# Optimization experiments

Measured on AMD Instinct MI355X. Metric: run time of the kernel, lower is better.

## Reference

```python
import jax, jax.numpy as jnp
import numpy as np

V, C, T_MAX, H, L = 32000, 256, 2048, 8, 4
HS = C // H          # head_size = 32
FFN = 256            # hard-coded in Encoder
CLS_H, N_OUT = 512, 10
B, T = 4, 2048
EPS = 1e-5


def _ln(x, g, b):
    mu = jnp.mean(x, axis=-1, keepdims=True)
    var = jnp.mean(jnp.square(x - mu), axis=-1, keepdims=True)
    return (x - mu) * jax.lax.rsqrt(var + EPS) * g + b


def setup_inputs() -> dict:
    key = jax.random.key(0)
    ks = jax.random.split(key, 16)
    s = 0.02
    return {
        "idx": jax.random.randint(ks[0], (B, T), 0, V),
        "tok_emb": jax.random.normal(ks[1], (V, C), jnp.float32) * s,
        "pos_emb": jax.random.normal(ks[2], (T_MAX, C), jnp.float32) * s,
        "Wq": jax.random.normal(ks[3], (L, H, C, HS), jnp.float32) * s,
        "Wk": jax.random.normal(ks[4], (L, H, C, HS), jnp.float32) * s,
        "Wv": jax.random.normal(ks[5], (L, H, C, HS), jnp.float32) * s,
        "Wproj": jax.random.normal(ks[6], (L, C, C), jnp.float32) * s,
        "bproj": jnp.zeros((L, C), jnp.float32),
        "ln1_g": jnp.ones((L, C), jnp.float32), "ln1_b": jnp.zeros((L, C), jnp.float32),
        "ln2_g": jnp.ones((L, C), jnp.float32), "ln2_b": jnp.zeros((L, C), jnp.float32),
        "W1": jax.random.normal(ks[7], (L, C, FFN), jnp.float32) * s,
        "b1": jnp.zeros((L, FFN), jnp.float32),
        "W2": jax.random.normal(ks[8], (L, FFN, C), jnp.float32) * s,
        "b2": jnp.zeros((L, C), jnp.float32),
        "lnf_g": jnp.ones((C,), jnp.float32), "lnf_b": jnp.zeros((C,), jnp.float32),
        "Wc1": jax.random.normal(ks[9], (C, CLS_H), jnp.float32) * s,
        "bc1": jnp.zeros((CLS_H,), jnp.float32),
        "Wc2": jax.random.normal(ks[10], (CLS_H, N_OUT), jnp.float32) * s,
        "bc2": jnp.zeros((N_OUT,), jnp.float32),
    }


def reference(idx, tok_emb, pos_emb, Wq, Wk, Wv, Wproj, bproj,
              ln1_g, ln1_b, ln2_g, ln2_b, W1, b1, W2, b2,
              lnf_g, lnf_b, Wc1, bc1, Wc2, bc2):
    Bc, Tc = idx.shape
    x = tok_emb[idx] + pos_emb[:Tc]                       # [B,T,C]
    scale = C ** (-0.5)                                   # NOTE: scales by n_embd, not head_size (faithful)
    for i in range(L):
        h = _ln(x, ln1_g[i], ln1_b[i])
        q = jnp.einsum('btc,hcd->bhtd', h, Wq[i])
        k = jnp.einsum('btc,hcd->bhtd', h, Wk[i])
        v = jnp.einsum('btc,hcd->bhtd', h, Wv[i])
        wei = jax.nn.softmax(jnp.einsum('bhtd,bhsd->bhts', q, k) * scale, axis=-1)
        o = jnp.einsum('bhts,bhsd->bhtd', wei, v)         # [B,H,T,HS]
        o = o.transpose(0, 2, 1, 3).reshape(Bc, Tc, C)    # concat heads
        x = x + jnp.einsum('btc,cd->btd', o, Wproj[i]) + bproj[i]
        h2 = _ln(x, ln2_g[i], ln2_b[i])
        f = jax.nn.relu(jnp.einsum('btc,cf->btf', h2, W1[i]) + b1[i])
        x = x + jnp.einsum('btf,fc->btc', f, W2[i]) + b2[i]
    x = _ln(x, lnf_g, lnf_b)
    emb = jnp.mean(x, axis=1)                             # [B,C] mean pool over T
    logits = jax.nn.relu(emb @ Wc1 + bc1) @ Wc2 + bc2
    return jax.nn.softmax(logits, axis=1)                 # [B, n_output]
```

## Files before the change

kernel.cpp:

```cpp
#include <hip/hip_runtime.h>
#include <hip/hip_bf16.h>

#define NTOK 8192
#define CDIM 256
#define TDIM 2048
#define BDIM 4
#define HDIM 8
#define HSZ  32
#define LNUM 4
#define BUF  (NTOK*CDIM)
#define QSTR 768
#define LC   0.0901684400056f

typedef __attribute__((ext_vector_type(8))) short short8v;
typedef __attribute__((ext_vector_type(4))) short short4v;
typedef __attribute__((ext_vector_type(4))) float float4v;

#if __has_builtin(__builtin_amdgcn_cvt_pk_bf16_f32)
static __device__ __forceinline__ unsigned pkbf(float a, float b){
  auto t = __builtin_amdgcn_cvt_pk_bf16_f32(a, b);
  union { decltype(t) v; unsigned u; } cv; cv.v = t;
  return cv.u;
}
static __device__ __forceinline__ short f2bs(float f){
  auto t = __builtin_amdgcn_cvt_pk_bf16_f32(f, f);
  union { decltype(t) v; unsigned u; } cv; cv.v = t;
  return (short)(cv.u & 0xFFFFu);
}
#else
static __device__ __forceinline__ short f2bs(float f){
  union { float f; unsigned u; } x; x.f = f;
  unsigned r = x.u + 0x7FFFu + ((x.u >> 16) & 1u);
  return (short)(r >> 16);
}
static __device__ __forceinline__ unsigned pkbf(float a, float b){
  union { float f; unsigned u; } x, y; x.f = a; y.f = b;
  unsigned ra = x.u + 0x7FFFu + ((x.u >> 16) & 1u);
  unsigned rb = y.u + 0x7FFFu + ((y.u >> 16) & 1u);
  return __builtin_amdgcn_perm(rb, ra, 0x07060302u);
}
#endif
#if __has_builtin(__builtin_amdgcn_exp2f)
static __device__ __forceinline__ float fexp2(float x){ return __builtin_amdgcn_exp2f(x); }
#else
static __device__ __forceinline__ float fexp2(float x){ return __expf(x*0.6931471805599453f); }
#endif

#if __has_builtin(__builtin_amdgcn_mfma_f32_16x16x16bf16_1k)
static __device__ __forceinline__ float4v mfma16(short4v a, short4v b, float4v c){
  return __builtin_amdgcn_mfma_f32_16x16x16bf16_1k(a, b, c, 0, 0, 0);
}
#else
static __device__ __forceinline__ float4v mfma16(short4v a, short4v b, float4v c){
  float4v d;
  asm volatile("v_mfma_f32_16x16x16_bf16 %0, %1, %2, %3\n\ts_nop 7\n\ts_nop 7"
               : "=v"(d) : "v"(a), "v"(b), "v"(c));
  return d;
}
#endif
static __device__ __forceinline__ float4v mfma32(short8v a, short8v b, float4v c){
  return __builtin_amdgcn_mfma_f32_16x16x32_bf16(a, b, c, 0, 0, 0);
}

__global__ __launch_bounds__(256) void k_prep_embed(
    const int* __restrict__ idx, const float* __restrict__ tok, const float* __restrict__ pos,
    const float* __restrict__ Wq, const float* __restrict__ Wk, const float* __restrict__ Wv,
    const float* __restrict__ Wp, const float* __restrict__ W1, const float* __restrict__ W2,
    const float* __restrict__ l1g, const float* __restrict__ l2g,
    const float* __restrict__ l1b, const float* __restrict__ l2b,
    const float* __restrict__ b1, const float* __restrict__ Wc1, const float* __restrict__ lnfg,
    const float* __restrict__ lnfb, const float* __restrict__ bc1,
    short* __restrict__ qkvT, short* __restrict__ wpT, short* __restrict__ w1T, short* __restrict__ w2T,
    float* __restrict__ bq, float* __restrict__ b1f, float* __restrict__ Wc1s, float* __restrict__ bc1f,
    float* __restrict__ x, short* __restrict__ y) {
  const int tid = threadIdx.x;
  const int id = blockIdx.x;
  if (id >= 513) {
    const int bid = id - 513;
    const int lane = tid & 63;
    const int bt = bid*4 + (tid >> 6);
    const int t = bt & (TDIM-1);
    float4 tv = *(const float4*)&tok[(size_t)idx[bt]*CDIM + lane*4];
    float4 pv = *(const float4*)&pos[(size_t)t*CDIM + lane*4];
    float4 v = make_float4(tv.x+pv.x, tv.y+pv.y, tv.z+pv.z, tv.w+pv.w);
    *(float4*)&x[(size_t)bt*CDIM + lane*4] = v;
    float s1 = (v.x+v.y) + (v.z+v.w);
    float s2 = fmaf(v.x,v.x, fmaf(v.y,v.y, fmaf(v.z,v.z, v.w*v.w)));
    #pragma unroll
    for (int off=32; off>0; off>>=1) { s1 += __shfl_xor(s1, off, 64); s2 += __shfl_xor(s2, off, 64); }
    float mean = s1*(1.f/CDIM);
    float inv  = rsqrtf(s2*(1.f/CDIM) - mean*mean + 1e-5f);
    float cc = -mean*inv;
    union { unsigned u[2]; short4v s; } o;
    o.u[0] = pkbf(fmaf(v.x,inv,cc), fmaf(v.y,inv,cc));
    o.u[1] = pkbf(fmaf(v.z,inv,cc), fmaf(v.w,inv,cc));
    *(short4v*)&y[(size_t)bt*CDIM + lane*4] = o.s;
    return;
  }
  if (id < 384) {
    __shared__ float tile[64][65];
    int l = id / 96, rr = id % 96;
    const float* src; short* dst; int n0, k0; bool qkvmode; int gsel; float nscale = 1.f;
    if (rr < 48) {
      int tn = rr >> 2, tk = rr & 3;
      n0 = tn*64; k0 = tk*64;
      const float* b3 = (n0 < 256) ? Wq : (n0 < 512 ? Wk : Wv);
      src = b3 + l*65536;
      dst = qkvT + (size_t)l*QSTR*256;
      qkvmode = true; gsel = 1;
      if (n0 < 256) nscale = LC;
    } else {
      int r2 = rr - 48;
      int mat = r2 >> 4, t = r2 & 15;
      int tn = t >> 2, tk = t & 3;
      n0 = tn*64; k0 = tk*64;
      const float* b3 = (mat == 0) ? Wp : (mat == 1 ? W1 : W2);
      src = b3 + l*65536;
      dst = (mat == 0 ? wpT : (mat == 1 ? w1T : w2T)) + l*65536;
      qkvmode = false; gsel = (mat == 1) ? 2 : 0;
    }
    const int cn = tid & 63, rk = tid >> 6;
    #pragma unroll
    for (int i = 0; i < 16; ++i) {
      int kk = rk + i*4;
      int n = n0 + cn, k = k0 + kk;
      float v;
      if (qkvmode) { int nn = n & 255; v = src[((nn>>5)*256 + k)*32 + (nn & 31)]; }
      else         { v = src[k*256 + n]; }
      if (gsel == 1)      v *= l1g[l*256 + k];
      else if (gsel == 2) v *= l2g[l*256 + k];
      tile[kk][cn] = v;
    }
    __syncthreads();
    #pragma unroll
    for (int i = 0; i < 16; ++i) {
      int nn = rk + i*4;
      dst[(size_t)(n0 + nn)*256 + k0 + cn] = f2bs(tile[cn][nn] * nscale);
    }
  } else if (id < 448) {
    __shared__ float red[4][64];
    int bid = id - 384;
    int l = bid >> 4, seg = bid & 15;
    int o = seg*64 + (tid & 63), pp = tid >> 6;
    float s = 0.f;
    if (o < 768) {
      const float* W = (o < 256 ? Wq : (o < 512 ? Wk : Wv)) + l*65536;
      int nn = o & 255, h = nn >> 5, d = nn & 31;
      const float* bv = l1b + l*256;
      for (int k = pp*64; k < pp*64+64; ++k) s = fmaf(bv[k], W[(h*256 + k)*32 + d], s);
    } else {
      const float* W = W1 + l*65536;
      int n = o - 768;
      const float* bv = l2b + l*256;
      for (int k = pp*64; k < pp*64+64; ++k) s = fmaf(bv[k], W[k*256 + n], s);
    }
    red[pp][tid & 63] = s;
    __syncthreads();
    if (tid < 64) {
      float tot = red[0][tid]+red[1][tid]+red[2][tid]+red[3][tid];
      int oo = seg*64 + tid;
      if (oo < 768) bq[l*768 + oo] = tot * (oo < 256 ? LC : 1.f);
      else          b1f[l*256 + (oo-768)] = b1[l*256 + (oo-768)] + tot;
    }
  } else if (id < 512) {
    int base = (id-448)*2048;
    #pragma unroll
    for (int i=0;i<8;++i) {
      int idx2 = base + i*256 + tid;
      Wc1s[idx2] = Wc1[idx2] * lnfg[idx2 >> 9];
    }
  } else {
    for (int u = tid; u < 512; u += 256) {
      float s = bc1[u];
      for (int k=0;k<256;++k) s = fmaf(lnfb[k], Wc1[k*512+u], s);
      bc1f[u] = s;
    }
  }
}

template<int NF, bool BIAS, bool RELU, bool OUTBF16, bool ACCUM>
__global__ __launch_bounds__(64) void k_gemm3(const short* __restrict__ A,
    const short* __restrict__ Bt, const float* __restrict__ bias, void* __restrict__ Cv,
    int outstride) {
  const int lane = threadIdx.x;
  const int q4 = lane >> 4, r = lane & 15;
  const int blockRow = blockIdx.x * 32;
  const int blockCol = blockIdx.y * (NF*16);
  float4v acc[2][NF];
  #pragma unroll
  for (int i=0;i<2;++i)
    #pragma unroll
    for (int j=0;j<NF;++j) acc[i][j] = (float4v){0,0,0,0};
  #pragma unroll
  for (int k0 = 0; k0 < 256; k0 += 32) {
    short8v a0 = *(const short8v*)&A[(size_t)(blockRow +      r)*CDIM + k0 + q4*8];
    short8v a1 = *(const short8v*)&A[(size_t)(blockRow + 16 + r)*CDIM + k0 + q4*8];
    #pragma unroll
    for (int nf=0; nf<NF; ++nf) {
      short8v bf = *(const short8v*)&Bt[(size_t)(blockCol + nf*16 + r)*256 + k0 + q4*8];
      acc[0][nf] = mfma32(a0, bf, acc[0][nf]);
      acc[1][nf] = mfma32(a1, bf, acc[1][nf]);
    }
  }
  #pragma unroll
  for (int mf=0; mf<2; ++mf)
    #pragma unroll
    for (int nf=0; nf<NF; ++nf) {
      int col = blockCol + nf*16 + r;
      float bb = BIAS ? bias[col] : 0.f;
      #pragma unroll
      for (int reg=0; reg<4; ++reg) {
        int row = blockRow + mf*16 + q4*4 + reg;
        float v = acc[mf][nf][reg] + bb;
        if (RELU) v = fmaxf(v, 0.f);
        size_t oi = (size_t)row*outstride + col;
        if (ACCUM)        ((float*)Cv)[oi] += v;
        else if (OUTBF16) ((short*)Cv)[oi] = f2bs(v);
        else              ((float*)Cv)[oi] = v;
      }
    }
}

template<bool LAST>
__global__ __launch_bounds__(1024, 4) void k_mlp(
    const short* __restrict__ A,
    const short* __restrict__ Bt,
    const float* __restrict__ bias,
    const short* __restrict__ W1t, const float* __restrict__ b1f,
    const short* __restrict__ W2t, const float* __restrict__ b2,
    float* __restrict__ X,
    const short* __restrict__ Wqkv,
    const float* __restrict__ bq,
    short* __restrict__ Qout) {
  __shared__ __align__(16) short Ys[32*264];
  __shared__ __align__(16) short Gs[32*264];
  __shared__ float S1[32][8], S2[32][8];
  const int tid = threadIdx.x;
  const int w = tid >> 6, lane = tid & 63;
  const int q4 = lane >> 4, r = lane & 15;
  const int wm = w & 1, wn = w >> 1;
  const int row0 = blockIdx.x * 32 + wm*16;
  const int col0 = wn*32;
  float4v acc[2];

  acc[0] = (float4v){0,0,0,0}; acc[1] = (float4v){0,0,0,0};
  #pragma unroll
  for (int k0 = 0; k0 < 256; k0 += 32) {
    short8v a0 = *(const short8v*)&A[(size_t)(row0 + r)*CDIM + k0 + q4*8];
    #pragma unroll
    for (int nf=0; nf<2; ++nf) {
      short8v bf = *(const short8v*)&Bt[(size_t)(col0 + nf*16 + r)*256 + k0 + q4*8];
      acc[nf] = mfma32(a0, bf, acc[nf]);
    }
  }
  {
    float v[2][4];
    float sw1[4], sw2[4];
    #pragma unroll
    for (int reg=0; reg<4; ++reg) {
      int row = row0 + q4*4 + reg;
      float s1 = 0.f, s2 = 0.f;
      #pragma unroll
      for (int nf=0; nf<2; ++nf) {
        int col = col0 + nf*16 + r;
        float t = acc[nf][reg] + bias[col] + X[(size_t)row*CDIM + col];
        v[nf][reg] = t;
        X[(size_t)row*CDIM + col] = t;
        s1 += t; s2 = fmaf(t, t, s2);
      }
      #pragma unroll
      for (int off=1; off<16; off<<=1) { s1 += __shfl_xor(s1, off, 64); s2 += __shfl_xor(s2, off, 64); }
      sw1[reg] = s1; sw2[reg] = s2;
    }
    if (r == 0) {
      #pragma unroll
      for (int reg=0; reg<4; ++reg) {
        S1[wm*16 + q4*4 + reg][wn] = sw1[reg];
        S2[wm*16 + q4*4 + reg][wn] = sw2[reg];
      }
    }
    __syncthreads();
    #pragma unroll
    for (int reg=0; reg<4; ++reg) {
      int ri = wm*16 + q4*4 + reg;
      float s1 = ((S1[ri][0]+S1[ri][1]) + (S1[ri][2]+S1[ri][3]))
               + ((S1[ri][4]+S1[ri][5]) + (S1[ri][6]+S1[ri][7]));
      float s2 = ((S2[ri][0]+S2[ri][1]) + (S2[ri][2]+S2[ri][3]))
               + ((S2[ri][4]+S2[ri][5]) + (S2[ri][6]+S2[ri][7]));
      float mean = s1*(1.f/CDIM);
      float inv  = rsqrtf(s2*(1.f/CDIM) - mean*mean + 1e-5f);
      float cc = -mean*inv;
      #pragma unroll
      for (int nf=0; nf<2; ++nf) {
        int col = col0 + nf*16 + r;
        Ys[ri*264 + col] = f2bs(fmaf(v[nf][reg], inv, cc));
      }
    }
  }
  __syncthreads();

  acc[0] = (float4v){0,0,0,0}; acc[1] = (float4v){0,0,0,0};
  #pragma unroll
  for (int k0 = 0; k0 < 256; k0 += 32) {
    short8v a0 = *(const short8v*)&Ys[(wm*16 + r)*264 + k0 + q4*8];
    #pragma unroll
    for (int nf=0; nf<2; ++nf) {
      short8v bf = *(const short8v*)&W1t[(size_t)(col0 + nf*16 + r)*256 + k0 + q4*8];
      acc[nf] = mfma32(a0, bf, acc[nf]);
    }
  }
  #pragma unroll
  for (int nf=0; nf<2; ++nf) {
    int col = col0 + nf*16 + r;
    float bb = b1f[col];
    #pragma unroll
    for (int reg=0; reg<4; ++reg) {
      int rl = wm*16 + q4*4 + reg;
      Gs[rl*264 + col] = f2bs(fmaxf(acc[nf][reg] + bb, 0.f));
    }
  }
  __syncthreads();
  acc[0] = (float4v){0,0,0,0}; acc[1] = (float4v){0,0,0,0};
  #pragma unroll
  for (int k0 = 0; k0 < 256; k0 += 32) {
    short8v a0 = *(const short8v*)&Gs[(wm*16 + r)*264 + k0 + q4*8];
    #pragma unroll
    for (int nf=0; nf<2; ++nf) {
      short8v bf = *(const short8v*)&W2t[(size_t)(col0 + nf*16 + r)*256 + k0 + q4*8];
      acc[nf] = mfma32(a0, bf, acc[nf]);
    }
  }
  {
    float v[2][4];
    float sw1[4], sw2[4];
    #pragma unroll
    for (int reg=0; reg<4; ++reg) {
      int row = row0 + q4*4 + reg;
      float s1 = 0.f, s2 = 0.f;
      #pragma unroll
      for (int nf=0; nf<2; ++nf) {
        int col = col0 + nf*16 + r;
        float t = acc[nf][reg] + b2[col] + X[(size_t)row*CDIM + col];
        v[nf][reg] = t;
        X[(size_t)row*CDIM + col] = t;
        s1 += t; s2 = fmaf(t, t, s2);
      }
      if (!LAST) {
        #pragma unroll
        for (int off=1; off<16; off<<=1) { s1 += __shfl_xor(s1, off, 64); s2 += __shfl_xor(s2, off, 64); }
        sw1[reg] = s1; sw2[reg] = s2;
      }
    }
    if (LAST) return;
    if (r == 0) {
      #pragma unroll
      for (int reg=0; reg<4; ++reg) {
        S1[wm*16 + q4*4 + reg][wn] = sw1[reg];
        S2[wm*16 + q4*4 + reg][wn] = sw2[reg];
      }
    }
    __syncthreads();
    #pragma unroll
    for (int reg=0; reg<4; ++reg) {
      int ri = wm*16 + q4*4 + reg;
      float s1 = ((S1[ri][0]+S1[ri][1]) + (S1[ri][2]+S1[ri][3]))
               + ((S1[ri][4]+S1[ri][5]) + (S1[ri][6]+S1[ri][7]));
      float s2 = ((S2[ri][0]+S2[ri][1]) + (S2[ri][2]+S2[ri][3]))
               + ((S2[ri][4]+S2[ri][5]) + (S2[ri][6]+S2[ri][7]));
      float mean = s1*(1.f/CDIM);
      float inv  = rsqrtf(s2*(1.f/CDIM) - mean*mean + 1e-5f);
      float cc = -mean*inv;
      #pragma unroll
      for (int nf=0; nf<2; ++nf) {
        int col = col0 + nf*16 + r;
        Ys[ri*264 + col] = f2bs(fmaf(v[nf][reg], inv, cc));
      }
    }
  }
  __syncthreads();

  {
    const int cb = w*48;
    float4v qa[2][3];
    #pragma unroll
    for (int i=0;i<2;++i)
      #pragma unroll
      for (int j=0;j<3;++j) qa[i][j] = (float4v){0,0,0,0};
    #pragma unroll
    for (int k0 = 0; k0 < 256; k0 += 32) {
      short8v a0 = *(const short8v*)&Ys[(     r)*264 + k0 + q4*8];
      short8v a1 = *(const short8v*)&Ys[(16 + r)*264 + k0 + q4*8];
      #pragma unroll
      for (int nf=0; nf<3; ++nf) {
        short8v bf = *(const short8v*)&Wqkv[(size_t)(cb + nf*16 + r)*256 + k0 + q4*8];
        qa[0][nf] = mfma32(a0, bf, qa[0][nf]);
        qa[1][nf] = mfma32(a1, bf, qa[1][nf]);
      }
    }
    #pragma unroll
    for (int mf=0; mf<2; ++mf)
      #pragma unroll
      for (int nf=0; nf<3; ++nf) {
        int col = cb + nf*16 + r;
        float bb = bq[col];
        #pragma unroll
        for (int reg=0; reg<4; ++reg) {
          int row = blockIdx.x*32 + mf*16 + q4*4 + reg;
          Qout[(size_t)row*QSTR + col] = f2bs(qa[mf][nf][reg] + bb);
        }
      }
  }
}

#define KSS 40
#define VTS 140
__global__ __launch_bounds__(512) void k_attn6(const short* __restrict__ qkv,
    short* __restrict__ O) {
  __shared__ __align__(16) short Ks[2][128*KSS];
  __shared__ __align__(16) short Vt[2][32*VTS];
  const int tid = threadIdx.x;
  const int w = tid >> 6, lane = tid & 63;
  const int q4 = lane >> 4, r = lane & 15;
  const int b = blockIdx.z, h = blockIdx.y;
  const int rowbase = blockIdx.x*128 + w*16;
  short8v Qf = *(const short8v*)&qkv[((size_t)(b*TDIM + rowbase + r))*QSTR + h*HSZ + q4*8];
  float4v o0 = {0,0,0,0}, o1 = {0,0,0,0};
  float l0 = 0.f;
  const bool isV = tid >= 256;
  const int t2 = tid & 255;
  const int kkey = t2 >> 1, kd0 = (t2 & 1)*16;
  const int kp = t2 & 63, dg = t2 >> 6;
  const short* kvbase = qkv + (size_t)b*TDIM*QSTR + h*HSZ;
  short8v ka, kb2, va, vb;
  if (isV) {
    va = *(const short8v*)&kvbase[(size_t)(2*kp)*QSTR   + 2*CDIM + dg*8];
    vb = *(const short8v*)&kvbase[(size_t)(2*kp+1)*QSTR + 2*CDIM + dg*8];
  } else {
    ka  = *(const short8v*)&kvbase[(size_t)kkey*QSTR + CDIM + kd0];
    kb2 = *(const short8v*)&kvbase[(size_t)kkey*QSTR + CDIM + kd0 + 8];
  }
  int p = 0;
  for (int s0 = 0; s0 < TDIM; s0 += 128, p ^= 1) {
    if (isV) {
      union { short8v s; unsigned u[4]; } A, C;
      A.s = va; C.s = vb;
      #pragma unroll
      for (int j=0;j<4;++j) {
        *(unsigned*)&Vt[p][(dg*8+2*j  )*VTS + 2*kp] = __builtin_amdgcn_perm(C.u[j], A.u[j], 0x05040100u);
        *(unsigned*)&Vt[p][(dg*8+2*j+1)*VTS + 2*kp] = __builtin_amdgcn_perm(C.u[j], A.u[j], 0x07060302u);
      }
    } else {
      *(short8v*)&Ks[p][kkey*KSS + kd0]     = ka;
      *(short8v*)&Ks[p][kkey*KSS + kd0 + 8] = kb2;
    }
    if (s0 + 128 < TDIM) {
      const short* nb = kvbase + (size_t)(s0+128)*QSTR;
      if (isV) {
        va = *(const short8v*)&nb[(size_t)(2*kp)*QSTR   + 2*CDIM + dg*8];
        vb = *(const short8v*)&nb[(size_t)(2*kp+1)*QSTR + 2*CDIM + dg*8];
      } else {
        ka  = *(const short8v*)&nb[(size_t)kkey*QSTR + CDIM + kd0];
        kb2 = *(const short8v*)&nb[(size_t)kkey*QSTR + CDIM + kd0 + 8];
      }
    }
    __syncthreads();
    #pragma unroll
    for (int ks = 0; ks < 8; ++ks) {
      short8v Kf = *(const short8v*)&Ks[p][(ks*16 + r)*KSS + q4*8];
      float4v sv = mfma32(Kf, Qf, (float4v){0,0,0,0});
      short4v Vf0 = *(const short4v*)&Vt[p][r*VTS + ks*16 + q4*4];
      short4v Vf1 = *(const short4v*)&Vt[p][(16+r)*VTS + ks*16 + q4*4];
      float p0 = fexp2(sv[0]), p1 = fexp2(sv[1]);
      float p2 = fexp2(sv[2]), p3 = fexp2(sv[3]);
      l0 += (p0+p1) + (p2+p3);
      union { unsigned u[2]; short4v s; } P;
      P.u[0] = pkbf(p0, p1); P.u[1] = pkbf(p2, p3);
      o0 = mfma16(P.s, Vf0, o0);
      o1 = mfma16(P.s, Vf1, o1);
    }
  }
  l0 += __shfl_xor(l0, 16, 64); l0 += __shfl_xor(l0, 32, 64);
  #pragma unroll
  for (int reg=0; reg<4; ++reg) {
    int qrow = q4*4 + reg;
    float i0 = 1.f / __shfl(l0, qrow, 64);
    short* op = O + ((size_t)(b*TDIM + rowbase + qrow))*CDIM + h*HSZ;
    op[r]    = f2bs(o0[reg]*i0);
    op[16+r] = f2bs(o1[reg]*i0);
  }
}

__global__ __launch_bounds__(256) void k_poolln(const float* __restrict__ X, float* __restrict__ part) {
  __shared__ float red[4][256];
  int b = blockIdx.x >> 3, chunk = blockIdx.x & 7;
  int wv = threadIdx.x >> 6, lane = threadIdx.x & 63;
  int base = b*TDIM + chunk*256 + wv*64;
  float a0=0,a1=0,a2=0,a3=0;
  for (int rr=0; rr<64; ++rr) {
    float4 v = *(const float4*)&X[(size_t)(base+rr)*CDIM + lane*4];
    float s1 = (v.x+v.y)+(v.z+v.w);
    float s2 = fmaf(v.x,v.x, fmaf(v.y,v.y, fmaf(v.z,v.z, v.w*v.w)));
    #pragma unroll
    for (int off=32; off>0; off>>=1) { s1 += __shfl_xor(s1,off,64); s2 += __shfl_xor(s2,off,64); }
    float mean = s1*(1.f/256.f);
    float inv  = rsqrtf(s2*(1.f/256.f) - mean*mean + 1e-5f);
    a0 = fmaf(v.x-mean, inv, a0); a1 = fmaf(v.y-mean, inv, a1);
    a2 = fmaf(v.z-mean, inv, a2); a3 = fmaf(v.w-mean, inv, a3);
  }
  red[wv][lane*4+0]=a0; red[wv][lane*4+1]=a1; red[wv][lane*4+2]=a2; red[wv][lane*4+3]=a3;
  __syncthreads();
  int c = threadIdx.x;
  part[blockIdx.x*256 + c] = (red[0][c]+red[1][c]+red[2][c]+red[3][c]) * (1.f/2048.f);
}

__global__ __launch_bounds__(512) void k_cls(const float* __restrict__ part,
    const float* __restrict__ Wc1s, const float* __restrict__ bc1f,
    const float* __restrict__ Wc2, const float* __restrict__ bc2, float* __restrict__ out) {
  __shared__ float se[4][256];
  __shared__ float sh[4][512];
  __shared__ float red[160];
  __shared__ float sl[40];
  const int t = threadIdx.x;
  for (int j=t; j<1024; j+=512) {
    int b = j >> 8, c = j & 255;
    float s = 0.f;
    #pragma unroll
    for (int ch=0; ch<8; ++ch) s += part[(b*8+ch)*256 + c];
    se[b][c] = s;
  }
  __syncthreads();
  {
    float bb = bc1f[t];
    float a0=bb, a1=bb, a2=bb, a3=bb;
    for (int c=0; c<256; ++c) {
      float w2 = Wc1s[c*512 + t];
      a0 = fmaf(se[0][c], w2, a0); a1 = fmaf(se[1][c], w2, a1);
      a2 = fmaf(se[2][c], w2, a2); a3 = fmaf(se[3][c], w2, a3);
    }
    sh[0][t]=fmaxf(a0,0.f); sh[1][t]=fmaxf(a1,0.f);
    sh[2][t]=fmaxf(a2,0.f); sh[3][t]=fmaxf(a3,0.f);
  }
  __syncthreads();
  if (t < 160) {
    int o = t >> 2, pp = t & 3;
    int b = o / 10, j = o - b*10;
    const float* hp = &sh[b][pp*128];
    float s = 0.f;
    #pragma unroll 8
    for (int u=0; u<128; ++u) s = fmaf(hp[u], Wc2[(pp*128+u)*10 + j], s);
    red[t] = s;
  }
  __syncthreads();
  if (t < 40) sl[t] = (red[t*4]+red[t*4+1]) + (red[t*4+2]+red[t*4+3]) + bc2[t%10];
  __syncthreads();
  if (t < 4) {
    float mx = -1e30f;
    for (int j=0;j<10;++j) mx = fmaxf(mx, sl[t*10+j]);
    float e[10], sum = 0.f;
    for (int j=0;j<10;++j) { e[j] = __expf(sl[t*10+j]-mx); sum += e[j]; }
    float inv = 1.f/sum;
    for (int j=0;j<10;++j) out[t*10+j] = e[j]*inv;
  }
}

extern "C" void kernel_launch(void* const* d_in, const int* in_sizes, int n_in,
                              void* d_out, int out_size, void* d_ws, size_t ws_size,
                              hipStream_t stream) {
  const int*   idx = (const int*)d_in[0];
  const float* tok = (const float*)d_in[1];
  const float* pos = (const float*)d_in[2];
  const float* Wq  = (const float*)d_in[3];
  const float* Wk  = (const float*)d_in[4];
  const float* Wv  = (const float*)d_in[5];
  const float* Wp  = (const float*)d_in[6];
  const float* bp  = (const float*)d_in[7];
  const float* l1g = (const float*)d_in[8];
  const float* l1b = (const float*)d_in[9];
  const float* l2g = (const float*)d_in[10];
  const float* l2b = (const float*)d_in[11];
  const float* W1  = (const float*)d_in[12];
  const float* b1  = (const float*)d_in[13];
  const float* W2  = (const float*)d_in[14];
  const float* b2  = (const float*)d_in[15];
  const float* lfg = (const float*)d_in[16];
  const float* lfb = (const float*)d_in[17];
  const float* Wc1 = (const float*)d_in[18];
  const float* bc1 = (const float*)d_in[19];
  const float* Wc2 = (const float*)d_in[20];
  const float* bc2 = (const float*)d_in[21];

  char* p = (char*)d_ws;
  float* xb   = (float*)p;              p += (size_t)BUF*4;
  short* hb   = (short*)p;              p += (size_t)BUF*2;
  short* qkvb = (short*)p;              p += (size_t)NTOK*QSTR*2;
  float* part = (float*)p;              p += 32*256*4;
  short* wqkvT = (short*)p;             p += (size_t)LNUM*QSTR*256*2;
  short* wpT   = (short*)p;             p += (size_t)LNUM*65536*2;
  short* w1T   = (short*)p;             p += (size_t)LNUM*65536*2;
  short* w2T   = (short*)p;             p += (size_t)LNUM*65536*2;
  float* bq    = (float*)p;             p += (size_t)LNUM*768*4;
  float* b1f   = (float*)p;             p += (size_t)LNUM*256*4;
  float* Wc1s  = (float*)p;             p += (size_t)256*512*4;
  float* bc1f  = (float*)p;             p += 512*4;

  k_prep_embed<<<513 + NTOK/4, 256, 0, stream>>>(idx, tok, pos,
                                   Wq, Wk, Wv, Wp, W1, W2, l1g, l2g, l1b, l2b,
                                   b1, Wc1, lfg, lfb, bc1,
                                   wqkvT, wpT, w1T, w2T, bq, b1f, Wc1s, bc1f,
                                   xb, hb);
  k_gemm3<4,true,false,true,false><<<dim3(256,12), 64, 0, stream>>>(
      hb, wqkvT, bq, qkvb, QSTR);
  for (int l = 0; l < LNUM; ++l) {
    k_attn6<<<dim3(16, HDIM, BDIM), 512, 0, stream>>>(qkvb, hb);
    if (l < LNUM-1) {
      k_mlp<false><<<256, 1024, 0, stream>>>(
          hb, wpT + (size_t)l*65536, bp + l*CDIM,
          w1T + (size_t)l*65536, b1f + l*CDIM, w2T + (size_t)l*65536, b2 + l*CDIM,
          xb,
          wqkvT + (size_t)(l+1)*QSTR*256, bq + (l+1)*768, qkvb);
    } else {
      k_mlp<true><<<256, 1024, 0, stream>>>(
          hb, wpT + (size_t)l*65536, bp + l*CDIM,
          w1T + (size_t)l*65536, b1f + l*CDIM, w2T + (size_t)l*65536, b2 + l*CDIM,
          xb,
          wqkvT, bq, qkvb);
    }
  }
  k_poolln<<<32, 256, 0, stream>>>(xb, part);
  k_cls<<<1, 512, 0, stream>>>(part, Wc1s, bc1f, Wc2, bc2, (float*)d_out);
}
```

Baseline: 512.1 us.

## Shrink fused MLP blocks to 16 rows with 512 threads, keep residual in registers

```diff
diff --git a/kernel.cpp b/kernel.cpp
--- a/kernel.cpp
+++ b/kernel.cpp
@@ -222,7 +222,7 @@
 }
 
 template<bool LAST>
-__global__ __launch_bounds__(1024, 4) void k_mlp(
+__global__ __launch_bounds__(512, 4) void k_mlp(
     const short* __restrict__ A,
     const short* __restrict__ Bt,
     const float* __restrict__ bias,
@@ -232,29 +232,27 @@
     const short* __restrict__ Wqkv,
     const float* __restrict__ bq,
     short* __restrict__ Qout) {
-  __shared__ __align__(16) short Ys[32*264];
-  __shared__ __align__(16) short Gs[32*264];
-  __shared__ float S1[32][8], S2[32][8];
+  __shared__ __align__(16) short Ys[16*264];
+  __shared__ __align__(16) short Gs[16*264];
+  __shared__ float S1[16][8], S2[16][8];
   const int tid = threadIdx.x;
   const int w = tid >> 6, lane = tid & 63;
   const int q4 = lane >> 4, r = lane & 15;
-  const int wm = w & 1, wn = w >> 1;
-  const int row0 = blockIdx.x * 32 + wm*16;
-  const int col0 = wn*32;
+  const int row0 = blockIdx.x * 16;
+  const int col0 = w*32;
   float4v acc[2];
+  float xv[2][4];
 
   acc[0] = (float4v){0,0,0,0}; acc[1] = (float4v){0,0,0,0};
   #pragma unroll
-  for (int k0 = 0; k0 < 256; k0 += 32) {
-    short8v a0 = *(const short8v*)&A[(size_t)(row0 + r)*CDIM + k0 + q4*8];
-    #pragma unroll
-    for (int nf=0; nf<2; ++nf) {
-      short8v bf = *(const short8v*)&Bt[(size_t)(col0 + nf*16 + r)*256 + k0 + q4*8];
-      acc[nf] = mfma32(a0, bf, acc[nf]);
-    }
+  for (int k=0;k<8;++k) {
+    short8v a0 = *(const short8v*)&A[(size_t)(row0 + r)*CDIM + k*32 + q4*8];
+    short8v b0 = *(const short8v*)&Bt[(size_t)(col0 +      r)*256 + k*32 + q4*8];
+    short8v b1r= *(const short8v*)&Bt[(size_t)(col0 + 16 + r)*256 + k*32 + q4*8];
+    acc[0] = mfma32(a0, b0,  acc[0]);
+    acc[1] = mfma32(a0, b1r, acc[1]);
   }
   {
-    float v[2][4];
     float sw1[4], sw2[4];
     #pragma unroll
     for (int reg=0; reg<4; ++reg) {
@@ -264,8 +262,7 @@
       for (int nf=0; nf<2; ++nf) {
         int col = col0 + nf*16 + r;
         float t = acc[nf][reg] + bias[col] + X[(size_t)row*CDIM + col];
-        v[nf][reg] = t;
-        X[(size_t)row*CDIM + col] = t;
+        xv[nf][reg] = t;
         s1 += t; s2 = fmaf(t, t, s2);
       }
       #pragma unroll
@@ -275,14 +272,14 @@
     if (r == 0) {
       #pragma unroll
       for (int reg=0; reg<4; ++reg) {
-        S1[wm*16 + q4*4 + reg][wn] = sw1[reg];
-        S2[wm*16 + q4*4 + reg][wn] = sw2[reg];
+        S1[q4*4 + reg][w] = sw1[reg];
+        S2[q4*4 + reg][w] = sw2[reg];
       }
     }
     __syncthreads();
     #pragma unroll
     for (int reg=0; reg<4; ++reg) {
-      int ri = wm*16 + q4*4 + reg;
+      int ri = q4*4 + reg;
       float s1 = ((S1[ri][0]+S1[ri][1]) + (S1[ri][2]+S1[ri][3]))
                + ((S1[ri][4]+S1[ri][5]) + (S1[ri][6]+S1[ri][7]));
       float s2 = ((S2[ri][0]+S2[ri][1]) + (S2[ri][2]+S2[ri][3]))
@@ -293,7 +290,7 @@
       #pragma unroll
       for (int nf=0; nf<2; ++nf) {
         int col = col0 + nf*16 + r;
-        Ys[ri*264 + col] = f2bs(fmaf(v[nf][reg], inv, cc));
+        Ys[ri*264 + col] = f2bs(fmaf(xv[nf][reg], inv, cc));
       }
     }
   }
@@ -301,13 +298,12 @@
 
   acc[0] = (float4v){0,0,0,0}; acc[1] = (float4v){0,0,0,0};
   #pragma unroll
-  for (int k0 = 0; k0 < 256; k0 += 32) {
-    short8v a0 = *(const short8v*)&Ys[(wm*16 + r)*264 + k0 + q4*8];
-    #pragma unroll
-    for (int nf=0; nf<2; ++nf) {
-      short8v bf = *(const short8v*)&W1t[(size_t)(col0 + nf*16 + r)*256 + k0 + q4*8];
-      acc[nf] = mfma32(a0, bf, acc[nf]);
-    }
+  for (int k=0;k<8;++k) {
+    short8v a0 = *(const short8v*)&Ys[(r)*264 + k*32 + q4*8];
+    short8v b0 = *(const short8v*)&W1t[(size_t)(col0 +      r)*256 + k*32 + q4*8];
+    short8v b1r= *(const short8v*)&W1t[(size_t)(col0 + 16 + r)*256 + k*32 + q4*8];
+    acc[0] = mfma32(a0, b0,  acc[0]);
+    acc[1] = mfma32(a0, b1r, acc[1]);
   }
   #pragma unroll
   for (int nf=0; nf<2; ++nf) {
@@ -315,23 +311,21 @@
     float bb = b1f[col];
     #pragma unroll
     for (int reg=0; reg<4; ++reg) {
-      int rl = wm*16 + q4*4 + reg;
+      int rl = q4*4 + reg;
       Gs[rl*264 + col] = f2bs(fmaxf(acc[nf][reg] + bb, 0.f));
     }
   }
   __syncthreads();
   acc[0] = (float4v){0,0,0,0}; acc[1] = (float4v){0,0,0,0};
   #pragma unroll
-  for (int k0 = 0; k0 < 256; k0 += 32) {
-    short8v a0 = *(const short8v*)&Gs[(wm*16 + r)*264 + k0 + q4*8];
-    #pragma unroll
-    for (int nf=0; nf<2; ++nf) {
-      short8v bf = *(const short8v*)&W2t[(size_t)(col0 + nf*16 + r)*256 + k0 + q4*8];
-      acc[nf] = mfma32(a0, bf, acc[nf]);
-    }
+  for (int k=0;k<8;++k) {
+    short8v a0 = *(const short8v*)&Gs[(r)*264 + k*32 + q4*8];
+    short8v b0 = *(const short8v*)&W2t[(size_t)(col0 +      r)*256 + k*32 + q4*8];
+    short8v b1r= *(const short8v*)&W2t[(size_t)(col0 + 16 + r)*256 + k*32 + q4*8];
+    acc[0] = mfma32(a0, b0,  acc[0]);
+    acc[1] = mfma32(a0, b1r, acc[1]);
   }
   {
-    float v[2][4];
     float sw1[4], sw2[4];
     #pragma unroll
     for (int reg=0; reg<4; ++reg) {
@@ -340,8 +334,8 @@
       #pragma unroll
       for (int nf=0; nf<2; ++nf) {
         int col = col0 + nf*16 + r;
-        float t = acc[nf][reg] + b2[col] + X[(size_t)row*CDIM + col];
-        v[nf][reg] = t;
+        float t = acc[nf][reg] + b2[col] + xv[nf][reg];
+        xv[nf][reg] = t;
         X[(size_t)row*CDIM + col] = t;
         s1 += t; s2 = fmaf(t, t, s2);
       }
@@ -355,14 +349,14 @@
     if (r == 0) {
       #pragma unroll
       for (int reg=0; reg<4; ++reg) {
-        S1[wm*16 + q4*4 + reg][wn] = sw1[reg];
-        S2[wm*16 + q4*4 + reg][wn] = sw2[reg];
+        S1[q4*4 + reg][w] = sw1[reg];
+        S2[q4*4 + reg][w] = sw2[reg];
       }
     }
     __syncthreads();
     #pragma unroll
     for (int reg=0; reg<4; ++reg) {
-      int ri = wm*16 + q4*4 + reg;
+      int ri = q4*4 + reg;
       float s1 = ((S1[ri][0]+S1[ri][1]) + (S1[ri][2]+S1[ri][3]))
                + ((S1[ri][4]+S1[ri][5]) + (S1[ri][6]+S1[ri][7]));
       float s2 = ((S2[ri][0]+S2[ri][1]) + (S2[ri][2]+S2[ri][3]))
@@ -373,42 +367,36 @@
       #pragma unroll
       for (int nf=0; nf<2; ++nf) {
         int col = col0 + nf*16 + r;
-        Ys[ri*264 + col] = f2bs(fmaf(v[nf][reg], inv, cc));
+        Ys[ri*264 + col] = f2bs(fmaf(xv[nf][reg], inv, cc));
       }
     }
   }
   __syncthreads();
 
   {
-    const int cb = w*48;
-    float4v qa[2][3];
-    #pragma unroll
-    for (int i=0;i<2;++i)
-      #pragma unroll
-      for (int j=0;j<3;++j) qa[i][j] = (float4v){0,0,0,0};
-    #pragma unroll
-    for (int k0 = 0; k0 < 256; k0 += 32) {
-      short8v a0 = *(const short8v*)&Ys[(     r)*264 + k0 + q4*8];
-      short8v a1 = *(const short8v*)&Ys[(16 + r)*264 + k0 + q4*8];
-      #pragma unroll
-      for (int nf=0; nf<3; ++nf) {
-        short8v bf = *(const short8v*)&Wqkv[(size_t)(cb + nf*16 + r)*256 + k0 + q4*8];
-        qa[0][nf] = mfma32(a0, bf, qa[0][nf]);
-        qa[1][nf] = mfma32(a1, bf, qa[1][nf]);
-      }
-    }
-    #pragma unroll
-    for (int mf=0; mf<2; ++mf)
-      #pragma unroll
-      for (int nf=0; nf<3; ++nf) {
-        int col = cb + nf*16 + r;
-        float bb = bq[col];
-        #pragma unroll
-        for (int reg=0; reg<4; ++reg) {
-          int row = blockIdx.x*32 + mf*16 + q4*4 + reg;
-          Qout[(size_t)row*QSTR + col] = f2bs(qa[mf][nf][reg] + bb);
-        }
-      }
+    const int cb = w*96;
+    float4v qa[6];
+    #pragma unroll
+    for (int j=0;j<6;++j) qa[j] = (float4v){0,0,0,0};
+    #pragma unroll
+    for (int k=0;k<8;++k) {
+      short8v a0 = *(const short8v*)&Ys[(r)*264 + k*32 + q4*8];
+      #pragma unroll
+      for (int nf=0; nf<6; ++nf) {
+        short8v bf = *(const short8v*)&Wqkv[(size_t)(cb + nf*16 + r)*256 + k*32 + q4*8];
+        qa[nf] = mfma32(a0, bf, qa[nf]);
+      }
+    }
+    #pragma unroll
+    for (int nf=0; nf<6; ++nf) {
+      int col = cb + nf*16 + r;
+      float bb = bq[col];
+      #pragma unroll
+      for (int reg=0; reg<4; ++reg) {
+        int row = row0 + q4*4 + reg;
+        Qout[(size_t)row*QSTR + col] = f2bs(qa[nf][reg] + bb);
+      }
+    }
   }
 }
 
@@ -613,13 +601,13 @@
   for (int l = 0; l < LNUM; ++l) {
     k_attn6<<<dim3(16, HDIM, BDIM), 512, 0, stream>>>(qkvb, hb);
     if (l < LNUM-1) {
-      k_mlp<false><<<256, 1024, 0, stream>>>(
+      k_mlp<false><<<512, 512, 0, stream>>>(
           hb, wpT + (size_t)l*65536, bp + l*CDIM,
           w1T + (size_t)l*65536, b1f + l*CDIM, w2T + (size_t)l*65536, b2 + l*CDIM,
           xb,
           wqkvT + (size_t)(l+1)*QSTR*256, bq + (l+1)*768, qkvb);
     } else {
-      k_mlp<true><<<256, 1024, 0, stream>>>(
+      k_mlp<true><<<512, 512, 0, stream>>>(
           hb, wpT + (size_t)l*65536, bp + l*CDIM,
           w1T + (size_t)l*65536, b1f + l*CDIM, w2T + (size_t)l*65536, b2 + l*CDIM,
           xb,
```

Result: slower. 532.4 us (+4.0%).

## Prefetch weight fragments in registers ahead of each GEMM stage in fused block kernel

Applied to the files above, without the earlier changes.

```diff
diff --git a/kernel.cpp b/kernel.cpp
--- a/kernel.cpp
+++ b/kernel.cpp
@@ -61,6 +61,7 @@
 static __device__ __forceinline__ float4v mfma32(short8v a, short8v b, float4v c){
   return __builtin_amdgcn_mfma_f32_16x16x32_bf16(a, b, c, 0, 0, 0);
 }
+static __device__ __forceinline__ void sbar(){ __builtin_amdgcn_sched_barrier(0); }
 
 __global__ __launch_bounds__(256) void k_prep_embed(
     const int* __restrict__ idx, const float* __restrict__ tok, const float* __restrict__ pos,
@@ -241,33 +242,46 @@
   const int wm = w & 1, wn = w >> 1;
   const int row0 = blockIdx.x * 32 + wm*16;
   const int col0 = wn*32;
-  float4v acc[2];
-
-  acc[0] = (float4v){0,0,0,0}; acc[1] = (float4v){0,0,0,0};
-  #pragma unroll
-  for (int k0 = 0; k0 < 256; k0 += 32) {
-    short8v a0 = *(const short8v*)&A[(size_t)(row0 + r)*CDIM + k0 + q4*8];
-    #pragma unroll
-    for (int nf=0; nf<2; ++nf) {
-      short8v bf = *(const short8v*)&Bt[(size_t)(col0 + nf*16 + r)*256 + k0 + q4*8];
-      acc[nf] = mfma32(a0, bf, acc[nf]);
-    }
-  }
+
+  short8v a8[8], bA0[8], bA1[8];
+  #pragma unroll
+  for (int k=0;k<8;++k) {
+    a8[k]  = *(const short8v*)&A[(size_t)(row0 + r)*CDIM + k*32 + q4*8];
+    bA0[k] = *(const short8v*)&Bt[(size_t)(col0 +      r)*256 + k*32 + q4*8];
+    bA1[k] = *(const short8v*)&Bt[(size_t)(col0 + 16 + r)*256 + k*32 + q4*8];
+  }
+  float xr0[4], xr1[4];
+  #pragma unroll
+  for (int reg=0;reg<4;++reg) {
+    int row = row0 + q4*4 + reg;
+    xr0[reg] = X[(size_t)row*CDIM + col0 + r];
+    xr1[reg] = X[(size_t)row*CDIM + col0 + 16 + r];
+  }
+  float bb0 = bias[col0 + r], bb1 = bias[col0 + 16 + r];
+  sbar();
+  float4v acc0 = {0,0,0,0}, acc1 = {0,0,0,0};
+  #pragma unroll
+  for (int k=0;k<8;++k) { acc0 = mfma32(a8[k], bA0[k], acc0); acc1 = mfma32(a8[k], bA1[k], acc1); }
+
+  short8v bB0[8], bB1[8];
+  #pragma unroll
+  for (int k=0;k<8;++k) {
+    bB0[k] = *(const short8v*)&W1t[(size_t)(col0 +      r)*256 + k*32 + q4*8];
+    bB1[k] = *(const short8v*)&W1t[(size_t)(col0 + 16 + r)*256 + k*32 + q4*8];
+  }
+  float g0 = b1f[col0 + r], g1 = b1f[col0 + 16 + r];
+  sbar();
+
+  float xv0[4], xv1[4];
   {
-    float v[2][4];
     float sw1[4], sw2[4];
     #pragma unroll
     for (int reg=0; reg<4; ++reg) {
-      int row = row0 + q4*4 + reg;
-      float s1 = 0.f, s2 = 0.f;
-      #pragma unroll
-      for (int nf=0; nf<2; ++nf) {
-        int col = col0 + nf*16 + r;
-        float t = acc[nf][reg] + bias[col] + X[(size_t)row*CDIM + col];
-        v[nf][reg] = t;
-        X[(size_t)row*CDIM + col] = t;
-        s1 += t; s2 = fmaf(t, t, s2);
-      }
+      float t0 = acc0[reg] + bb0 + xr0[reg];
+      float t1 = acc1[reg] + bb1 + xr1[reg];
+      xv0[reg] = t0; xv1[reg] = t1;
+      float s1 = t0 + t1;
+      float s2 = fmaf(t0, t0, t1*t1);
       #pragma unroll
       for (int off=1; off<16; off<<=1) { s1 += __shfl_xor(s1, off, 64); s2 += __shfl_xor(s2, off, 64); }
       sw1[reg] = s1; sw2[reg] = s2;
@@ -290,62 +304,66 @@
       float mean = s1*(1.f/CDIM);
       float inv  = rsqrtf(s2*(1.f/CDIM) - mean*mean + 1e-5f);
       float cc = -mean*inv;
-      #pragma unroll
-      for (int nf=0; nf<2; ++nf) {
-        int col = col0 + nf*16 + r;
-        Ys[ri*264 + col] = f2bs(fmaf(v[nf][reg], inv, cc));
-      }
-    }
-  }
-  __syncthreads();
-
-  acc[0] = (float4v){0,0,0,0}; acc[1] = (float4v){0,0,0,0};
-  #pragma unroll
-  for (int k0 = 0; k0 < 256; k0 += 32) {
-    short8v a0 = *(const short8v*)&Ys[(wm*16 + r)*264 + k0 + q4*8];
-    #pragma unroll
-    for (int nf=0; nf<2; ++nf) {
-      short8v bf = *(const short8v*)&W1t[(size_t)(col0 + nf*16 + r)*256 + k0 + q4*8];
-      acc[nf] = mfma32(a0, bf, acc[nf]);
-    }
-  }
-  #pragma unroll
-  for (int nf=0; nf<2; ++nf) {
-    int col = col0 + nf*16 + r;
-    float bb = b1f[col];
-    #pragma unroll
-    for (int reg=0; reg<4; ++reg) {
-      int rl = wm*16 + q4*4 + reg;
-      Gs[rl*264 + col] = f2bs(fmaxf(acc[nf][reg] + bb, 0.f));
-    }
-  }
-  __syncthreads();
-  acc[0] = (float4v){0,0,0,0}; acc[1] = (float4v){0,0,0,0};
-  #pragma unroll
-  for (int k0 = 0; k0 < 256; k0 += 32) {
-    short8v a0 = *(const short8v*)&Gs[(wm*16 + r)*264 + k0 + q4*8];
-    #pragma unroll
-    for (int nf=0; nf<2; ++nf) {
-      short8v bf = *(const short8v*)&W2t[(size_t)(col0 + nf*16 + r)*256 + k0 + q4*8];
-      acc[nf] = mfma32(a0, bf, acc[nf]);
-    }
-  }
+      Ys[ri*264 + col0 + r]      = f2bs(fmaf(xv0[reg], inv, cc));
+      Ys[ri*264 + col0 + 16 + r] = f2bs(fmaf(xv1[reg], inv, cc));
+    }
+  }
+  __syncthreads();
+
+  acc0 = (float4v){0,0,0,0}; acc1 = (float4v){0,0,0,0};
+  #pragma unroll
+  for (int k=0;k<8;++k) {
+    short8v ay = *(const short8v*)&Ys[(wm*16 + r)*264 + k*32 + q4*8];
+    acc0 = mfma32(ay, bB0[k], acc0);
+    acc1 = mfma32(ay, bB1[k], acc1);
+  }
+  short8v bC0[8], bC1[8];
+  #pragma unroll
+  for (int k=0;k<8;++k) {
+    bC0[k] = *(const short8v*)&W2t[(size_t)(col0 +      r)*256 + k*32 + q4*8];
+    bC1[k] = *(const short8v*)&W2t[(size_t)(col0 + 16 + r)*256 + k*32 + q4*8];
+  }
+  float bb20 = b2[col0 + r], bb21 = b2[col0 + 16 + r];
+  sbar();
+  #pragma unroll
+  for (int reg=0; reg<4; ++reg) {
+    int rl = wm*16 + q4*4 + reg;
+    Gs[rl*264 + col0 + r]      = f2bs(fmaxf(acc0[reg] + g0, 0.f));
+    Gs[rl*264 + col0 + 16 + r] = f2bs(fmaxf(acc1[reg] + g1, 0.f));
+  }
+  __syncthreads();
+
+  acc0 = (float4v){0,0,0,0}; acc1 = (float4v){0,0,0,0};
+  #pragma unroll
+  for (int k=0;k<8;++k) {
+    short8v ag = *(const short8v*)&Gs[(wm*16 + r)*264 + k*32 + q4*8];
+    acc0 = mfma32(ag, bC0[k], acc0);
+    acc1 = mfma32(ag, bC1[k], acc1);
+  }
+  const int cb = w*48;
+  short8v qP0[9];
+  if (!LAST) {
+    #pragma unroll
+    for (int nf=0; nf<3; ++nf)
+      #pragma unroll
+      for (int k=0;k<3;++k)
+        qP0[nf*3+k] = *(const short8v*)&Wqkv[(size_t)(cb + nf*16 + r)*256 + k*32 + q4*8];
+  }
+  sbar();
+
   {
-    float v[2][4];
     float sw1[4], sw2[4];
     #pragma unroll
     for (int reg=0; reg<4; ++reg) {
       int row = row0 + q4*4 + reg;
-      float s1 = 0.f, s2 = 0.f;
-      #pragma unroll
-      for (int nf=0; nf<2; ++nf) {
-        int col = col0 + nf*16 + r;
-        float t = acc[nf][reg] + b2[col] + X[(size_t)row*CDIM + col];
-        v[nf][reg] = t;
-        X[(size_t)row*CDIM + col] = t;
-        s1 += t; s2 = fmaf(t, t, s2);
-      }
+      float t0 = acc0[reg] + bb20 + xv0[reg];
+      float t1 = acc1[reg] + bb21 + xv1[reg];
+      xv0[reg] = t0; xv1[reg] = t1;
+      X[(size_t)row*CDIM + col0 + r]      = t0;
+      X[(size_t)row*CDIM + col0 + 16 + r] = t1;
       if (!LAST) {
+        float s1 = t0 + t1;
+        float s2 = fmaf(t0, t0, t1*t1);
         #pragma unroll
         for (int off=1; off<16; off<<=1) { s1 += __shfl_xor(s1, off, 64); s2 += __shfl_xor(s2, off, 64); }
         sw1[reg] = s1; sw2[reg] = s2;
@@ -370,45 +388,71 @@
       float mean = s1*(1.f/CDIM);
       float inv  = rsqrtf(s2*(1.f/CDIM) - mean*mean + 1e-5f);
       float cc = -mean*inv;
-      #pragma unroll
-      for (int nf=0; nf<2; ++nf) {
-        int col = col0 + nf*16 + r;
-        Ys[ri*264 + col] = f2bs(fmaf(v[nf][reg], inv, cc));
-      }
+      Ys[ri*264 + col0 + r]      = f2bs(fmaf(xv0[reg], inv, cc));
+      Ys[ri*264 + col0 + 16 + r] = f2bs(fmaf(xv1[reg], inv, cc));
     }
   }
   __syncthreads();
 
   {
-    const int cb = w*48;
-    float4v qa[2][3];
-    #pragma unroll
-    for (int i=0;i<2;++i)
-      #pragma unroll
-      for (int j=0;j<3;++j) qa[i][j] = (float4v){0,0,0,0};
-    #pragma unroll
-    for (int k0 = 0; k0 < 256; k0 += 32) {
-      short8v a0 = *(const short8v*)&Ys[(     r)*264 + k0 + q4*8];
-      short8v a1 = *(const short8v*)&Ys[(16 + r)*264 + k0 + q4*8];
+    float4v qa0[3], qa1[3];
+    #pragma unroll
+    for (int j=0;j<3;++j) { qa0[j] = (float4v){0,0,0,0}; qa1[j] = (float4v){0,0,0,0}; }
+    short8v qP1[9];
+    #pragma unroll
+    for (int nf=0; nf<3; ++nf)
+      #pragma unroll
+      for (int k=0;k<3;++k)
+        qP1[nf*3+k] = *(const short8v*)&Wqkv[(size_t)(cb + nf*16 + r)*256 + (k+3)*32 + q4*8];
+    float bq0 = bq[cb + r], bq1 = bq[cb + 16 + r], bq2 = bq[cb + 32 + r];
+    sbar();
+    #pragma unroll
+    for (int k=0;k<3;++k) {
+      short8v ay0 = *(const short8v*)&Ys[(     r)*264 + k*32 + q4*8];
+      short8v ay1 = *(const short8v*)&Ys[(16 + r)*264 + k*32 + q4*8];
       #pragma unroll
       for (int nf=0; nf<3; ++nf) {
-        short8v bf = *(const short8v*)&Wqkv[(size_t)(cb + nf*16 + r)*256 + k0 + q4*8];
-        qa[0][nf] = mfma32(a0, bf, qa[0][nf]);
-        qa[1][nf] = mfma32(a1, bf, qa[1][nf]);
-      }
-    }
-    #pragma unroll
-    for (int mf=0; mf<2; ++mf)
+        qa0[nf] = mfma32(ay0, qP0[nf*3+k], qa0[nf]);
+        qa1[nf] = mfma32(ay1, qP0[nf*3+k], qa1[nf]);
+      }
+    }
+    short8v qP2[6];
+    #pragma unroll
+    for (int nf=0; nf<3; ++nf)
+      #pragma unroll
+      for (int k=0;k<2;++k)
+        qP2[nf*2+k] = *(const short8v*)&Wqkv[(size_t)(cb + nf*16 + r)*256 + (k+6)*32 + q4*8];
+    sbar();
+    #pragma unroll
+    for (int k=0;k<3;++k) {
+      short8v ay0 = *(const short8v*)&Ys[(     r)*264 + (k+3)*32 + q4*8];
+      short8v ay1 = *(const short8v*)&Ys[(16 + r)*264 + (k+3)*32 + q4*8];
       #pragma unroll
       for (int nf=0; nf<3; ++nf) {
-        int col = cb + nf*16 + r;
-        float bb = bq[col];
-        #pragma unroll
-        for (int reg=0; reg<4; ++reg) {
-          int row = blockIdx.x*32 + mf*16 + q4*4 + reg;
-          Qout[(size_t)row*QSTR + col] = f2bs(qa[mf][nf][reg] + bb);
-        }
-      }
+        qa0[nf] = mfma32(ay0, qP1[nf*3+k], qa0[nf]);
+        qa1[nf] = mfma32(ay1, qP1[nf*3+k], qa1[nf]);
+      }
+    }
+    #pragma unroll
+    for (int k=0;k<2;++k) {
+      short8v ay0 = *(const short8v*)&Ys[(     r)*264 + (k+6)*32 + q4*8];
+      short8v ay1 = *(const short8v*)&Ys[(16 + r)*264 + (k+6)*32 + q4*8];
+      #pragma unroll
+      for (int nf=0; nf<3; ++nf) {
+        qa0[nf] = mfma32(ay0, qP2[nf*2+k], qa0[nf]);
+        qa1[nf] = mfma32(ay1, qP2[nf*2+k], qa1[nf]);
+      }
+    }
+    float bqv[3] = {bq0, bq1, bq2};
+    #pragma unroll
+    for (int nf=0; nf<3; ++nf) {
+      int col = cb + nf*16 + r;
+      #pragma unroll
+      for (int reg=0; reg<4; ++reg) {
+        Qout[(size_t)(blockIdx.x*32      + q4*4 + reg)*QSTR + col] = f2bs(qa0[nf][reg] + bqv[nf]);
+        Qout[(size_t)(blockIdx.x*32 + 16 + q4*4 + reg)*QSTR + col] = f2bs(qa1[nf][reg] + bqv[nf]);
+      }
+    }
   }
 }
 
```

Result: no change. 519.7 us (+1.5%).
